# Performance work log

Measured on AMD Instinct MI355X. Metric: run time of the kernel, lower is better.

## Reference

```python
import jax, jax.numpy as jnp
import numpy as np

N = 50000          # atoms (nodes)
NEIGH = 12         # neighbors per atom
N_CRYS = 500       # crystals, 100 atoms each (contiguous)
H_E = 128          # h_fea_edge
H_A = 128          # h_fea_angle
N_CLS = 2
BOND_STEPS, BOND_MIN, BOND_MAX = 40, 0.0, 8.0
ANG_STEPS, ANG_MIN, ANG_MAX = 8, -1.0, 1.0


def _gbf(data, dmin, dmax, steps):
    # Gaussian basis expansion on the last (new) axis
    filters = jnp.linspace(dmin, dmax, steps, dtype=jnp.float32)
    gamma = (dmax - dmin) / steps
    return jnp.exp(-((data[..., None] - filters) ** 2) / (gamma ** 2))


def _sage_conv(x, src, dst, Wl, Wr, b):
    # PyG SAGEConv, mean aggregation:
    #   out_i = Wl @ mean_{(j->i) in E} x_j + b + Wr @ x_i
    n = x.shape[0]
    msg = x[src]                                             # [E, F] gather
    agg = jax.ops.segment_sum(msg, dst, num_segments=n)      # [N, F] scatter-add
    cnt = jax.ops.segment_sum(jnp.ones((src.shape[0],), x.dtype), dst, num_segments=n)
    agg = agg / jnp.maximum(cnt, 1.0)[:, None]
    return agg @ Wl.T + b + x @ Wr.T


def _segment_mean_pool(x, crys_idx):
    # crys_idx: [C, 2] contiguous [start, end) ranges covering [0, N)
    n = x.shape[0]
    starts = crys_idx[:, 0]
    seg_id = jnp.searchsorted(starts, jnp.arange(n), side='right') - 1
    counts = (crys_idx[:, 1] - crys_idx[:, 0]).astype(x.dtype)
    summed = jax.ops.segment_sum(x, seg_id, num_segments=crys_idx.shape[0])
    return summed / jnp.maximum(counts, 1.0)[:, None]


def setup_inputs() -> dict:
    key = jax.random.key(0)
    ks = jax.random.split(key, 24)
    in_b = BOND_STEPS * NEIGH            # 480
    in_a = ANG_STEPS * NEIGH * NEIGH     # 1152
    h_cat = H_E + H_A                    # 256

    def lin(k, fo, fi):
        return jax.random.normal(k, (fo, fi), jnp.float32) * (1.0 / np.sqrt(fi))

    atoms_per = N // N_CRYS
    starts = np.arange(N_CRYS, dtype=np.int32) * atoms_per
    crys_idx = jnp.asarray(np.stack([starts, starts + atoms_per], axis=1))

    return {
        'bond_fea': jax.random.uniform(ks[0], (N, NEIGH), jnp.float32) * BOND_MAX,
        'angle_fea': jax.random.uniform(ks[1], (N, NEIGH, NEIGH), jnp.float32) * 2.0 - 1.0,
        'species': jax.random.randint(ks[2], (N,), 0, 100, jnp.int32),
        'nbr_idx': jax.random.randint(ks[3], (N, NEIGH), 0, N, jnp.int32),
        'crys_idx': crys_idx,
        'Wl_b1': lin(ks[4], H_E, in_b), 'Wr_b1': lin(ks[5], H_E, in_b),
        'b_b1': jnp.zeros((H_E,), jnp.float32),
        'Wl_a1': lin(ks[6], H_A, in_a), 'Wr_a1': lin(ks[7], H_A, in_a),
        'b_a1': jnp.zeros((H_A,), jnp.float32),
        'Wl_b': jnp.stack([lin(ks[8], H_E, H_E), lin(ks[9], H_E, H_E)]),
        'Wr_b': jnp.stack([lin(ks[10], H_E, H_E), lin(ks[11], H_E, H_E)]),
        'b_b': jnp.zeros((2, H_E), jnp.float32),
        'Wl_a': jnp.stack([lin(ks[12], H_A, H_A), lin(ks[13], H_A, H_A)]),
        'Wr_a': jnp.stack([lin(ks[14], H_A, H_A), lin(ks[15], H_A, H_A)]),
        'b_a': jnp.zeros((2, H_A), jnp.float32),
        'W_mlp': jnp.stack([lin(ks[16], h_cat, h_cat), lin(ks[17], h_cat, h_cat)]),
        'b_mlp': jnp.zeros((2, h_cat), jnp.float32),
        'W_fc': lin(ks[18], N_CLS, h_cat),
        'b_fc': jnp.zeros((N_CLS,), jnp.float32),
    }


def reference(bond_fea, angle_fea, species, nbr_idx, crys_idx,
              Wl_b1, Wr_b1, b_b1, Wl_a1, Wr_a1, b_a1,
              Wl_b, Wr_b, b_b, Wl_a, Wr_a, b_a,
              W_mlp, b_mlp, W_fc, b_fc):
    n, neigh = nbr_idx.shape
    # get_edge_index: source = repeated node id, dest = neighbor id
    src = jnp.repeat(jnp.arange(n, dtype=nbr_idx.dtype), neigh)   # [N*neigh]
    dst = nbr_idx.reshape(-1)                                     # [N*neigh]

    # GBF expansions, flattened per node
    edge_fea = _gbf(bond_fea, BOND_MIN, BOND_MAX, BOND_STEPS).reshape(n, -1)    # [N, 480]
    ang_fea = _gbf(angle_fea, ANG_MIN, ANG_MAX, ANG_STEPS).reshape(n, -1)       # [N, 1152]

    # first SAGE layers (dropout_prob = 0 -> identity)
    b_out = jax.nn.relu(_sage_conv(edge_fea, src, dst, Wl_b1, Wr_b1, b_b1))
    a_out = jax.nn.relu(_sage_conv(ang_fea, src, dst, Wl_a1, Wr_a1, b_a1))

    # stacked SAGE layers (n_conv - 1 = 2 each)
    for i in range(Wl_b.shape[0]):
        b_out = jax.nn.relu(_sage_conv(b_out, src, dst, Wl_b[i], Wr_b[i], b_b[i]))
    for i in range(Wl_a.shape[0]):
        a_out = jax.nn.relu(_sage_conv(a_out, src, dst, Wl_a[i], Wr_a[i], b_a[i]))

    crys_fea = jnp.concatenate([b_out, a_out], axis=1)   # [N, 256]
    crys_fea = _segment_mean_pool(crys_fea, crys_idx)     # [C, 256]

    for i in range(W_mlp.shape[0]):
        crys_fea = crys_fea @ W_mlp[i].T + b_mlp[i]

    return crys_fea @ W_fc.T + b_fc                       # [C, n_classification]
```

## Files before the change

kernel.cpp:

```cpp
#include <hip/hip_runtime.h>

typedef _Float16 f16;
typedef _Float16 f16x8 __attribute__((ext_vector_type(8)));
typedef float f32x4 __attribute__((ext_vector_type(4)));

#define N_ATOMS 50000
#define NEIGH   12
#define NEDGE   (N_ATOMS * NEIGH)
#define NCRYS   500
#define NBLK    196

__device__ __forceinline__ void gld_lds16(const void* g, void* l) {
  __builtin_amdgcn_global_load_lds(
      (const __attribute__((address_space(1))) unsigned int*)g,
      (__attribute__((address_space(3))) unsigned int*)l, 16, 0, 0);
}

template <int MODE, int K>
__global__ __launch_bounds__(512) void gemm1(
    const float* __restrict__ Asrc, const f16* __restrict__ Wcat,
    f16* __restrict__ P, f16* __restrict__ Q, int n) {
  __shared__ __align__(16) f16 As[2][4][256][8];
  __shared__ __align__(16) f16 Bs[2][4][128][8];
  const int tid = threadIdx.x;
  const int lane = tid & 63;
  const int wid = tid >> 6;
  const int wr = wid >> 1;
  const int wc = wid & 1;
  const int row0 = blockIdx.x * 256;
  const int half = blockIdx.y;
  const f16* Wh = Wcat + (size_t)half * 128 * K;
  f16* outp = half ? Q : P;

  const int bcol = tid & 127;
  const int bkb = tid >> 7;
  const int sArow = tid & 255;
  const int sAkb0 = tid >> 8;
  int arow = row0 + sArow;
  if (arow >= n) arow = n - 1;

  f32x4 acc[4][4];
#pragma unroll
  for (int m = 0; m < 4; ++m)
#pragma unroll
    for (int q = 0; q < 4; ++q) acc[m][q] = (f32x4)0.f;

  auto stage = [&](int buf, int k0) {
    gld_lds16(Wh + (size_t)bcol * K + k0 + bkb * 8, &Bs[buf][bkb][bcol][0]);
#pragma unroll
    for (int p = 0; p < 2; ++p) {
      int kb = sAkb0 + 2 * p;
      int kg0 = k0 + kb * 8;
      f16 v[8];
      if constexpr (MODE == 1) {
        int jn = kg0 / 40;
        int kk0 = kg0 - jn * 40;
        float d = Asrc[arow * NEIGH + jn];
#pragma unroll
        for (int j = 0; j < 8; ++j) {
          float t = d - (kk0 + j) * (8.0f / 39.0f);
          v[j] = (f16)__expf(-t * t * 25.0f);
        }
      } else {
        int jn = kg0 >> 3;
        float d = Asrc[arow * 144 + jn];
#pragma unroll
        for (int j = 0; j < 8; ++j) {
          float t = d - (-1.0f + j * (2.0f / 7.0f));
          v[j] = (f16)__expf(-t * t * 16.0f);
        }
      }
      *(f16x8*)&As[buf][kb][sArow][0] = *(const f16x8*)v;
    }
  };

  constexpr int NT = K / 32;
  stage(0, 0);
  __syncthreads();
  int buf = 0;
  for (int t = 0; t < NT; ++t) {
    if (t + 1 < NT) stage(buf ^ 1, (t + 1) * 32);
    const int kb = lane >> 4;
    const int r16 = lane & 15;
    f16x8 a[4], b[4];
#pragma unroll
    for (int m = 0; m < 4; ++m)
      a[m] = *(const f16x8*)&As[buf][kb][wr * 64 + m * 16 + r16][0];
#pragma unroll
    for (int q = 0; q < 4; ++q)
      b[q] = *(const f16x8*)&Bs[buf][kb][wc * 64 + q * 16 + r16][0];
#pragma unroll
    for (int m = 0; m < 4; ++m)
#pragma unroll
      for (int q = 0; q < 4; ++q)
        acc[m][q] =
            __builtin_amdgcn_mfma_f32_16x16x32_f16(a[m], b[q], acc[m][q], 0, 0, 0);
    __syncthreads();
    buf ^= 1;
  }

  const int crow = (lane >> 4) * 4;
  const int ccol = lane & 15;
#pragma unroll
  for (int m = 0; m < 4; ++m) {
#pragma unroll
    for (int r = 0; r < 4; ++r) {
      int row = row0 + wr * 64 + m * 16 + crow + r;
      if (row < n) {
#pragma unroll
        for (int q = 0; q < 4; ++q)
          outp[(size_t)row * 128 + wc * 64 + q * 16 + ccol] = (f16)acc[m][q][r];
      }
    }
  }
}

__global__ __launch_bounds__(512) void gemmL(
    f16* __restrict__ axb, f16* __restrict__ axa, const f16* __restrict__ Wall,
    const float* __restrict__ bb, const float* __restrict__ ba, int lidx, int n) {
  __shared__ __align__(16) f16 As[2][4][256][8];
  __shared__ __align__(16) f16 Bs[2][4][128][8];
  const int path = blockIdx.y;
  f16* ax = path ? axa : axb;
  const f16* W = Wall + (size_t)(path * 2 + lidx) * 32768;
  const float* bias = (path ? ba : bb) + lidx * 128;

  const int tid = threadIdx.x;
  const int lane = tid & 63;
  const int wid = tid >> 6;
  const int wr = wid >> 1;
  const int wc = wid & 1;
  const int row0 = blockIdx.x * 256;

  const int bcol = tid & 127;
  const int bkb = tid >> 7;
  const int sArow = tid & 255;
  const int sAkb0 = tid >> 8;
  int arow = row0 + sArow;
  if (arow >= n) arow = n - 1;

  f32x4 acc[4][4];
#pragma unroll
  for (int m = 0; m < 4; ++m)
#pragma unroll
    for (int q = 0; q < 4; ++q) acc[m][q] = (f32x4)0.f;

  auto stage = [&](int buf, int k0) {
    gld_lds16(W + (size_t)bcol * 256 + k0 + bkb * 8, &Bs[buf][bkb][bcol][0]);
#pragma unroll
    for (int p = 0; p < 2; ++p) {
      int kb = sAkb0 + 2 * p;
      gld_lds16(ax + (size_t)arow * 256 + k0 + kb * 8, &As[buf][kb][sArow][0]);
    }
  };

  stage(0, 0);
  __syncthreads();
  int buf = 0;
  for (int t = 0; t < 8; ++t) {
    if (t + 1 < 8) stage(buf ^ 1, (t + 1) * 32);
    const int kb = lane >> 4;
    const int r16 = lane & 15;
    f16x8 a[4], b[4];
#pragma unroll
    for (int m = 0; m < 4; ++m)
      a[m] = *(const f16x8*)&As[buf][kb][wr * 64 + m * 16 + r16][0];
#pragma unroll
    for (int q = 0; q < 4; ++q)
      b[q] = *(const f16x8*)&Bs[buf][kb][wc * 64 + q * 16 + r16][0];
#pragma unroll
    for (int m = 0; m < 4; ++m)
#pragma unroll
      for (int q = 0; q < 4; ++q)
        acc[m][q] =
            __builtin_amdgcn_mfma_f32_16x16x32_f16(a[m], b[q], acc[m][q], 0, 0, 0);
    __syncthreads();
    buf ^= 1;
  }

  const int crow = (lane >> 4) * 4;
  const int ccol = lane & 15;
#pragma unroll
  for (int m = 0; m < 4; ++m) {
#pragma unroll
    for (int r = 0; r < 4; ++r) {
      int row = row0 + wr * 64 + m * 16 + crow + r;
      if (row < n) {
#pragma unroll
        for (int q = 0; q < 4; ++q) {
          int col = wc * 64 + q * 16 + ccol;
          float v = acc[m][q][r] + bias[col];
          ax[(size_t)row * 256 + 128 + col] = (f16)fmaxf(v, 0.0f);
        }
      }
    }
  }
}

__global__ void cvtW(const float* __restrict__ Wl, const float* __restrict__ Wr,
                     f16* __restrict__ outp, int K) {
  int c = blockIdx.y;
  int k = blockIdx.x * 256 + threadIdx.x;
  if (k < K)
    outp[(size_t)c * K + k] =
        (f16)((c < 128) ? Wl[(size_t)c * K + k] : Wr[(size_t)(c - 128) * K + k]);
}

__global__ void cvtW_small(const float* __restrict__ Wl_b, const float* __restrict__ Wr_b,
                           const float* __restrict__ Wl_a, const float* __restrict__ Wr_a,
                           f16* __restrict__ outp) {
  int idx = blockIdx.x * 256 + threadIdx.x;
  int l = idx >> 15;
  int c = (idx >> 8) & 127;
  int k = idx & 255;
  const float* Wl = (l < 2) ? Wl_b + (size_t)l * 16384 : Wl_a + (size_t)(l - 2) * 16384;
  const float* Wr = (l < 2) ? Wr_b + (size_t)l * 16384 : Wr_a + (size_t)(l - 2) * 16384;
  float v = (k < 128) ? Wl[(size_t)c * 128 + k] : Wr[(size_t)c * 128 + (k - 128)];
  outp[idx] = (f16)v;
}

__global__ void k_count(const int* __restrict__ nbr, int* __restrict__ deg) {
  int e = blockIdx.x * 256 + threadIdx.x;
  if (e < NEDGE) atomicAdd(&deg[nbr[e]], 1);
}
__global__ void k_scan1(const int* __restrict__ deg, int* __restrict__ rowptr,
                        int* __restrict__ bsum) {
  __shared__ int s[256];
  int t = threadIdx.x, i = blockIdx.x * 256 + t;
  int v = (i < N_ATOMS) ? deg[i] : 0;
  s[t] = v;
  __syncthreads();
  for (int off = 1; off < 256; off <<= 1) {
    int x = (t >= off) ? s[t - off] : 0;
    __syncthreads();
    s[t] += x;
    __syncthreads();
  }
  if (i < N_ATOMS) rowptr[i] = s[t] - v;
  if (t == 255) bsum[blockIdx.x] = s[255];
}
__global__ void k_scan2(int* __restrict__ bsum) {
  __shared__ int s[256];
  int t = threadIdx.x;
  int v = (t < NBLK) ? bsum[t] : 0;
  s[t] = v;
  __syncthreads();
  for (int off = 1; off < 256; off <<= 1) {
    int x = (t >= off) ? s[t - off] : 0;
    __syncthreads();
    s[t] += x;
    __syncthreads();
  }
  if (t < NBLK) bsum[t] = s[t] - v;
}
__global__ void k_scan3(int* __restrict__ rowptr, const int* __restrict__ bsum) {
  int i = blockIdx.x * 256 + threadIdx.x;
  if (i < N_ATOMS) rowptr[i] += bsum[blockIdx.x];
  if (i == 0) rowptr[N_ATOMS] = NEDGE;
}
__global__ void k_fill(const int* __restrict__ nbr, const int* __restrict__ rowptr,
                       int* __restrict__ cursor, int* __restrict__ eidx) {
  int e = blockIdx.x * 256 + threadIdx.x;
  if (e < NEDGE) {
    int dst = nbr[e];
    int pos = rowptr[dst] + atomicAdd(&cursor[dst], 1);
    eidx[pos] = e / NEIGH;
  }
}

__global__ __launch_bounds__(256) void gather_fin1(
    const f16* __restrict__ Pb, const f16* __restrict__ Qb,
    const f16* __restrict__ Pa, const f16* __restrict__ Qa,
    const int* __restrict__ rowptr, const int* __restrict__ eidx,
    const float* __restrict__ bias_b, const float* __restrict__ bias_a,
    f16* __restrict__ axb, f16* __restrict__ axa) {
  const int path = blockIdx.y;
  const f16* P = path ? Pa : Pb;
  const f16* Q = path ? Qa : Qb;
  const float* bias = path ? bias_a : bias_b;
  f16* ax = path ? axa : axb;
  const int t = threadIdx.x;
  const int a = blockIdx.x * 16 + (t >> 4);
  const int g = (t & 15) * 8;
  const int s0 = rowptr[a], s1 = rowptr[a + 1];
  float acc[8];
#pragma unroll
  for (int u = 0; u < 8; ++u) acc[u] = 0.f;
  int j = s0;
  for (; j + 4 <= s1; j += 4) {
    int src0 = eidx[j], src1 = eidx[j + 1], src2 = eidx[j + 2], src3 = eidx[j + 3];
    f16x8 v0 = *(const f16x8*)&P[(size_t)src0 * 128 + g];
    f16x8 v1 = *(const f16x8*)&P[(size_t)src1 * 128 + g];
    f16x8 v2 = *(const f16x8*)&P[(size_t)src2 * 128 + g];
    f16x8 v3 = *(const f16x8*)&P[(size_t)src3 * 128 + g];
#pragma unroll
    for (int u = 0; u < 8; ++u)
      acc[u] += ((float)v0[u] + (float)v1[u]) + ((float)v2[u] + (float)v3[u]);
  }
  for (; j < s1; ++j) {
    f16x8 v = *(const f16x8*)&P[(size_t)eidx[j] * 128 + g];
#pragma unroll
    for (int u = 0; u < 8; ++u) acc[u] += (float)v[u];
  }
  f16x8 q = *(const f16x8*)&Q[(size_t)a * 128 + g];
  float inv = 1.0f / fmaxf((float)(s1 - s0), 1.0f);
  f16 outv[8];
#pragma unroll
  for (int u = 0; u < 8; ++u) {
    float v = acc[u] * inv + bias[g + u] + (float)q[u];
    outv[u] = (f16)fmaxf(v, 0.0f);
  }
  *(f16x8*)&ax[(size_t)a * 256 + 128 + g] = *(const f16x8*)outv;
}

__global__ __launch_bounds__(256) void gather_mean(
    f16* __restrict__ axb, f16* __restrict__ axa,
    const int* __restrict__ rowptr, const int* __restrict__ eidx) {
  f16* ax = blockIdx.y ? axa : axb;
  const int t = threadIdx.x;
  const int a = blockIdx.x * 16 + (t >> 4);
  const int g = (t & 15) * 8;
  const int s0 = rowptr[a], s1 = rowptr[a + 1];
  float acc[8];
#pragma unroll
  for (int u = 0; u < 8; ++u) acc[u] = 0.f;
  int j = s0;
  for (; j + 4 <= s1; j += 4) {
    int src0 = eidx[j], src1 = eidx[j + 1], src2 = eidx[j + 2], src3 = eidx[j + 3];
    f16x8 v0 = *(const f16x8*)&ax[(size_t)src0 * 256 + 128 + g];
    f16x8 v1 = *(const f16x8*)&ax[(size_t)src1 * 256 + 128 + g];
    f16x8 v2 = *(const f16x8*)&ax[(size_t)src2 * 256 + 128 + g];
    f16x8 v3 = *(const f16x8*)&ax[(size_t)src3 * 256 + 128 + g];
#pragma unroll
    for (int u = 0; u < 8; ++u)
      acc[u] += ((float)v0[u] + (float)v1[u]) + ((float)v2[u] + (float)v3[u]);
  }
  for (; j < s1; ++j) {
    f16x8 v = *(const f16x8*)&ax[(size_t)eidx[j] * 256 + 128 + g];
#pragma unroll
    for (int u = 0; u < 8; ++u) acc[u] += (float)v[u];
  }
  float inv = 1.0f / fmaxf((float)(s1 - s0), 1.0f);
  f16 outv[8];
#pragma unroll
  for (int u = 0; u < 8; ++u) outv[u] = (f16)(acc[u] * inv);
  *(f16x8*)&ax[(size_t)a * 256 + g] = *(const f16x8*)outv;
}

__global__ __launch_bounds__(256) void head_kernel(
    const f16* __restrict__ axb, const f16* __restrict__ axa,
    const int* __restrict__ crys, const float* __restrict__ W_mlp,
    const float* __restrict__ b_mlp, const float* __restrict__ W_fc,
    const float* __restrict__ b_fc, float* __restrict__ outp) {
  __shared__ float sh0[256], sh1[256];
  const int cry = blockIdx.x, c = threadIdx.x;
  const int s = crys[2 * cry], e = crys[2 * cry + 1];
  const f16* src = (c < 128) ? axb : axa;
  const int ch = c & 127;
  float sum = 0.f;
  for (int r = s; r < e; ++r) sum += (float)src[(size_t)r * 256 + 128 + ch];
  sh0[c] = sum / fmaxf((float)(e - s), 1.0f);
  __syncthreads();
  {
    const float* wrow = W_mlp + (size_t)c * 256;
    float s2 = b_mlp[c];
#pragma unroll 8
    for (int k = 0; k < 256; k += 4) {
      float4 w = *(const float4*)&wrow[k];
      s2 += sh0[k] * w.x + sh0[k + 1] * w.y + sh0[k + 2] * w.z + sh0[k + 3] * w.w;
    }
    sh1[c] = s2;
  }
  __syncthreads();
  {
    const float* wrow = W_mlp + 65536 + (size_t)c * 256;
    float s2 = b_mlp[256 + c];
#pragma unroll 8
    for (int k = 0; k < 256; k += 4) {
      float4 w = *(const float4*)&wrow[k];
      s2 += sh1[k] * w.x + sh1[k + 1] * w.y + sh1[k + 2] * w.z + sh1[k + 3] * w.w;
    }
    sh0[c] = s2;
  }
  __syncthreads();
  if (c < 2) {
    const float* wrow = W_fc + c * 256;
    float s2 = b_fc[c];
    for (int k = 0; k < 256; ++k) s2 += sh0[k] * wrow[k];
    outp[cry * 2 + c] = s2;
  }
}

extern "C" void kernel_launch(void* const* d_in, const int* in_sizes, int n_in,
                              void* d_out, int out_size, void* d_ws, size_t ws_size,
                              hipStream_t stream) {
  const float* bond  = (const float*)d_in[0];
  const float* angle = (const float*)d_in[1];
  const int*   nbr   = (const int*)d_in[3];
  const int*   crys  = (const int*)d_in[4];
  const float* Wl_b1 = (const float*)d_in[5];
  const float* Wr_b1 = (const float*)d_in[6];
  const float* b_b1  = (const float*)d_in[7];
  const float* Wl_a1 = (const float*)d_in[8];
  const float* Wr_a1 = (const float*)d_in[9];
  const float* b_a1  = (const float*)d_in[10];
  const float* Wl_b  = (const float*)d_in[11];
  const float* Wr_b  = (const float*)d_in[12];
  const float* b_b   = (const float*)d_in[13];
  const float* Wl_a  = (const float*)d_in[14];
  const float* Wr_a  = (const float*)d_in[15];
  const float* b_a   = (const float*)d_in[16];
  const float* W_mlp = (const float*)d_in[17];
  const float* b_mlp = (const float*)d_in[18];
  const float* W_fc  = (const float*)d_in[19];
  const float* b_fc  = (const float*)d_in[20];

  char* w = (char*)d_ws;
  auto alloc = [&](size_t bytes) {
    void* p = (void*)w;
    w += (bytes + 255) & ~(size_t)255;
    return p;
  };
  f16* Pb   = (f16*)alloc((size_t)N_ATOMS * 128 * 2);
  f16* Qb   = (f16*)alloc((size_t)N_ATOMS * 128 * 2);
  f16* Pa   = (f16*)alloc((size_t)N_ATOMS * 128 * 2);
  f16* Qa   = (f16*)alloc((size_t)N_ATOMS * 128 * 2);
  f16* axb  = (f16*)alloc((size_t)N_ATOMS * 256 * 2);
  f16* axa  = (f16*)alloc((size_t)N_ATOMS * 256 * 2);
  f16* Wb1c = (f16*)alloc((size_t)256 * 480 * 2);
  f16* Wa1c = (f16*)alloc((size_t)256 * 1152 * 2);
  f16* Wsm  = (f16*)alloc((size_t)4 * 128 * 256 * 2);
  int* deg    = (int*)alloc((size_t)2 * N_ATOMS * 4);
  int* cursor = deg + N_ATOMS;
  int* rowptr = (int*)alloc((size_t)(N_ATOMS + 1) * 4);
  int* eidx   = (int*)alloc((size_t)NEDGE * 4);
  int* bsum   = (int*)alloc(256 * 4);

  cvtW<<<dim3(2, 256), 256, 0, stream>>>(Wl_b1, Wr_b1, Wb1c, 480);
  cvtW<<<dim3(5, 256), 256, 0, stream>>>(Wl_a1, Wr_a1, Wa1c, 1152);
  cvtW_small<<<512, 256, 0, stream>>>(Wl_b, Wr_b, Wl_a, Wr_a, Wsm);

  hipMemsetAsync(deg, 0, (size_t)2 * N_ATOMS * 4, stream);
  k_count<<<(NEDGE + 255) / 256, 256, 0, stream>>>(nbr, deg);
  k_scan1<<<NBLK, 256, 0, stream>>>(deg, rowptr, bsum);
  k_scan2<<<1, 256, 0, stream>>>(bsum);
  k_scan3<<<NBLK, 256, 0, stream>>>(rowptr, bsum);
  k_fill<<<(NEDGE + 255) / 256, 256, 0, stream>>>(nbr, rowptr, cursor, eidx);

  const int GT = (N_ATOMS + 255) / 256;
  const int AG = N_ATOMS / 16;

  gemm1<2, 1152><<<dim3(GT, 2), 512, 0, stream>>>(angle, Wa1c, Pa, Qa, N_ATOMS);
  gemm1<1, 480><<<dim3(GT, 2), 512, 0, stream>>>(bond, Wb1c, Pb, Qb, N_ATOMS);
  gather_fin1<<<dim3(AG, 2), 256, 0, stream>>>(Pb, Qb, Pa, Qa, rowptr, eidx,
                                               b_b1, b_a1, axb, axa);

  for (int l = 0; l < 2; ++l) {
    gather_mean<<<dim3(AG, 2), 256, 0, stream>>>(axb, axa, rowptr, eidx);
    gemmL<<<dim3(GT, 2), 512, 0, stream>>>(axb, axa, Wsm, b_b, b_a, l, N_ATOMS);
  }

  head_kernel<<<NCRYS, 256, 0, stream>>>(axb, axa, crys, W_mlp, b_mlp, W_fc, b_fc,
                                         (float*)d_out);
}
```

Before: 418.1 us.

## Replace LDS-staged GEMMs with register-direct MFMA loads and transposed inputs

Both first-layer and later GEMMs drop shared-memory double buffering and instead load A and B fragments directly from global memory into registers, prefetching one k-step ahead. The tile shrinks to 128 rows with 256 threads. Bond and angle inputs are first transposed to column-major so each lane's scalar loads coalesce across atoms. Later layers ping-pong between two activation buffers to avoid an in-place read/write hazard. This removes LDS traffic and barriers, at the cost of extra transpose kernels, redundant global loads of weights per wave, and more workspace.

```diff
diff --git a/kernel.cpp b/kernel.cpp
--- a/kernel.cpp
+++ b/kernel.cpp
@@ -10,34 +10,47 @@
 #define NCRYS   500
 #define NBLK    196
 
-__device__ __forceinline__ void gld_lds16(const void* g, void* l) {
-  __builtin_amdgcn_global_load_lds(
-      (const __attribute__((address_space(1))) unsigned int*)g,
-      (__attribute__((address_space(3))) unsigned int*)l, 16, 0, 0);
+template <int C>
+__global__ __launch_bounds__(256) void transposeT(const float* __restrict__ in,
+                                                  float* __restrict__ outp) {
+  __shared__ float tile[64 * C];
+  const int r0 = blockIdx.x * 64;
+  const int nr = min(64, N_ATOMS - r0);
+  for (int idx = threadIdx.x; idx < nr * C; idx += 256) {
+    int r = idx / C, c = idx - r * C;
+    tile[r * C + c] = in[(size_t)(r0 + r) * C + c];
+  }
+  __syncthreads();
+  for (int idx = threadIdx.x; idx < 64 * C; idx += 256) {
+    int c = idx >> 6, r = idx & 63;
+    if (r < nr) outp[(size_t)c * N_ATOMS + r0 + r] = tile[r * C + c];
+  }
 }
 
 template <int MODE, int K>
-__global__ __launch_bounds__(512) void gemm1(
-    const float* __restrict__ Asrc, const f16* __restrict__ Wcat,
+__global__ __launch_bounds__(256) void gemm1_reg(
+    const float* __restrict__ AT, const f16* __restrict__ Wcat,
     f16* __restrict__ P, f16* __restrict__ Q, int n) {
-  __shared__ __align__(16) f16 As[2][4][256][8];
-  __shared__ __align__(16) f16 Bs[2][4][128][8];
-  const int tid = threadIdx.x;
-  const int lane = tid & 63;
-  const int wid = tid >> 6;
-  const int wr = wid >> 1;
-  const int wc = wid & 1;
-  const int row0 = blockIdx.x * 256;
-  const int half = blockIdx.y;
-  const f16* Wh = Wcat + (size_t)half * 128 * K;
-  f16* outp = half ? Q : P;
-
-  const int bcol = tid & 127;
-  const int bkb = tid >> 7;
-  const int sArow = tid & 255;
-  const int sAkb0 = tid >> 8;
-  int arow = row0 + sArow;
-  if (arow >= n) arow = n - 1;
+  const int lane = threadIdx.x & 63;
+  const int wid = threadIdx.x >> 6;
+  const int wr = wid & 1;
+  const int wc = wid >> 1;
+  const int row0 = blockIdx.x * 128;
+  const f16* Wh = Wcat + (size_t)blockIdx.y * 128 * K;
+  f16* outp = blockIdx.y ? Q : P;
+  const int r16 = lane & 15;
+  const int kb = lane >> 4;
+
+  int rm[4];
+#pragma unroll
+  for (int m = 0; m < 4; ++m) {
+    int r = row0 + wr * 64 + m * 16 + r16;
+    rm[m] = (r < n) ? r : (n - 1);
+  }
+  const f16* wb[4];
+#pragma unroll
+  for (int q = 0; q < 4; ++q)
+    wb[q] = Wh + (size_t)(wc * 64 + q * 16 + r16) * K + kb * 8;
 
   f32x4 acc[4][4];
 #pragma unroll
@@ -45,58 +58,61 @@
 #pragma unroll
     for (int q = 0; q < 4; ++q) acc[m][q] = (f32x4)0.f;
 
-  auto stage = [&](int buf, int k0) {
-    gld_lds16(Wh + (size_t)bcol * K + k0 + bkb * 8, &Bs[buf][bkb][bcol][0]);
-#pragma unroll
-    for (int p = 0; p < 2; ++p) {
-      int kb = sAkb0 + 2 * p;
-      int kg0 = k0 + kb * 8;
-      f16 v[8];
-      if constexpr (MODE == 1) {
-        int jn = kg0 / 40;
-        int kk0 = kg0 - jn * 40;
-        float d = Asrc[arow * NEIGH + jn];
-#pragma unroll
-        for (int j = 0; j < 8; ++j) {
-          float t = d - (kk0 + j) * (8.0f / 39.0f);
-          v[j] = (f16)__expf(-t * t * 25.0f);
-        }
-      } else {
-        int jn = kg0 >> 3;
-        float d = Asrc[arow * 144 + jn];
-#pragma unroll
-        for (int j = 0; j < 8; ++j) {
-          float t = d - (-1.0f + j * (2.0f / 7.0f));
-          v[j] = (f16)__expf(-t * t * 16.0f);
-        }
+  constexpr int NT = K / 32;
+  float d0[4];
+  f16x8 b0[4];
+  {
+    int kg = kb * 8;
+    int jn = (MODE == 1) ? kg / 40 : (kg >> 3);
+#pragma unroll
+    for (int m = 0; m < 4; ++m) d0[m] = AT[(size_t)jn * N_ATOMS + rm[m]];
+#pragma unroll
+    for (int q = 0; q < 4; ++q) b0[q] = *(const f16x8*)(wb[q]);
+  }
+
+  for (int t = 0; t < NT; ++t) {
+    float d1[4];
+    f16x8 b1[4];
+    if (t + 1 < NT) {
+      int kg = (t + 1) * 32 + kb * 8;
+      int jn = (MODE == 1) ? kg / 40 : (kg >> 3);
+#pragma unroll
+      for (int m = 0; m < 4; ++m) d1[m] = AT[(size_t)jn * N_ATOMS + rm[m]];
+#pragma unroll
+      for (int q = 0; q < 4; ++q) b1[q] = *(const f16x8*)(wb[q] + (t + 1) * 32);
+    }
+    f16x8 a[4];
+    float fbase, fstep, g2i;
+    if constexpr (MODE == 1) {
+      int kg = t * 32 + kb * 8;
+      int jn = kg / 40;
+      fbase = (float)(kg - jn * 40) * (8.0f / 39.0f);
+      fstep = 8.0f / 39.0f;
+      g2i = 25.0f;
+    } else {
+      fbase = -1.0f;
+      fstep = 2.0f / 7.0f;
+      g2i = 16.0f;
+    }
+#pragma unroll
+    for (int m = 0; m < 4; ++m) {
+      float dd = d0[m];
+#pragma unroll
+      for (int j = 0; j < 8; ++j) {
+        float tt = dd - (fbase + (float)j * fstep);
+        a[m][j] = (f16)__expf(-tt * tt * g2i);
       }
-      *(f16x8*)&As[buf][kb][sArow][0] = *(const f16x8*)v;
-    }
-  };
-
-  constexpr int NT = K / 32;
-  stage(0, 0);
-  __syncthreads();
-  int buf = 0;
-  for (int t = 0; t < NT; ++t) {
-    if (t + 1 < NT) stage(buf ^ 1, (t + 1) * 32);
-    const int kb = lane >> 4;
-    const int r16 = lane & 15;
-    f16x8 a[4], b[4];
-#pragma unroll
-    for (int m = 0; m < 4; ++m)
-      a[m] = *(const f16x8*)&As[buf][kb][wr * 64 + m * 16 + r16][0];
-#pragma unroll
-    for (int q = 0; q < 4; ++q)
-      b[q] = *(const f16x8*)&Bs[buf][kb][wc * 64 + q * 16 + r16][0];
+    }
 #pragma unroll
     for (int m = 0; m < 4; ++m)
 #pragma unroll
       for (int q = 0; q < 4; ++q)
         acc[m][q] =
-            __builtin_amdgcn_mfma_f32_16x16x32_f16(a[m], b[q], acc[m][q], 0, 0, 0);
-    __syncthreads();
-    buf ^= 1;
+            __builtin_amdgcn_mfma_f32_16x16x32_f16(a[m], b0[q], acc[m][q], 0, 0, 0);
+#pragma unroll
+    for (int m = 0; m < 4; ++m) d0[m] = d1[m];
+#pragma unroll
+    for (int q = 0; q < 4; ++q) b0[q] = b1[q];
   }
 
   const int crow = (lane >> 4) * 4;
@@ -115,29 +131,34 @@
   }
 }
 
-__global__ __launch_bounds__(512) void gemmL(
-    f16* __restrict__ axb, f16* __restrict__ axa, const f16* __restrict__ Wall,
+__global__ __launch_bounds__(256) void gemmL_reg(
+    const f16* __restrict__ srcB, const f16* __restrict__ srcA,
+    f16* __restrict__ dstB, f16* __restrict__ dstA, const f16* __restrict__ Wall,
     const float* __restrict__ bb, const float* __restrict__ ba, int lidx, int n) {
-  __shared__ __align__(16) f16 As[2][4][256][8];
-  __shared__ __align__(16) f16 Bs[2][4][128][8];
   const int path = blockIdx.y;
-  f16* ax = path ? axa : axb;
+  const f16* src = path ? srcA : srcB;
+  f16* dst = path ? dstA : dstB;
   const f16* W = Wall + (size_t)(path * 2 + lidx) * 32768;
   const float* bias = (path ? ba : bb) + lidx * 128;
 
-  const int tid = threadIdx.x;
-  const int lane = tid & 63;
-  const int wid = tid >> 6;
-  const int wr = wid >> 1;
-  const int wc = wid & 1;
-  const int row0 = blockIdx.x * 256;
-
-  const int bcol = tid & 127;
-  const int bkb = tid >> 7;
-  const int sArow = tid & 255;
-  const int sAkb0 = tid >> 8;
-  int arow = row0 + sArow;
-  if (arow >= n) arow = n - 1;
+  const int lane = threadIdx.x & 63;
+  const int wid = threadIdx.x >> 6;
+  const int wr = wid & 1;
+  const int wc = wid >> 1;
+  const int row0 = blockIdx.x * 128;
+  const int r16 = lane & 15;
+  const int kb = lane >> 4;
+
+  int rm[4];
+#pragma unroll
+  for (int m = 0; m < 4; ++m) {
+    int r = row0 + wr * 64 + m * 16 + r16;
+    rm[m] = (r < n) ? r : (n - 1);
+  }
+  const f16* wb[4];
+#pragma unroll
+  for (int q = 0; q < 4; ++q)
+    wb[q] = W + (size_t)(wc * 64 + q * 16 + r16) * 256 + kb * 8;
 
   f32x4 acc[4][4];
 #pragma unroll
@@ -145,37 +166,33 @@
 #pragma unroll
     for (int q = 0; q < 4; ++q) acc[m][q] = (f32x4)0.f;
 
-  auto stage = [&](int buf, int k0) {
-    gld_lds16(W + (size_t)bcol * 256 + k0 + bkb * 8, &Bs[buf][bkb][bcol][0]);
-#pragma unroll
-    for (int p = 0; p < 2; ++p) {
-      int kb = sAkb0 + 2 * p;
-      gld_lds16(ax + (size_t)arow * 256 + k0 + kb * 8, &As[buf][kb][sArow][0]);
-    }
-  };
-
-  stage(0, 0);
-  __syncthreads();
-  int buf = 0;
+  f16x8 a0[4], b0[4];
+#pragma unroll
+  for (int m = 0; m < 4; ++m)
+    a0[m] = *(const f16x8*)&src[(size_t)rm[m] * 256 + kb * 8];
+#pragma unroll
+  for (int q = 0; q < 4; ++q) b0[q] = *(const f16x8*)(wb[q]);
+
   for (int t = 0; t < 8; ++t) {
-    if (t + 1 < 8) stage(buf ^ 1, (t + 1) * 32);
-    const int kb = lane >> 4;
-    const int r16 = lane & 15;
-    f16x8 a[4], b[4];
-#pragma unroll
-    for (int m = 0; m < 4; ++m)
-      a[m] = *(const f16x8*)&As[buf][kb][wr * 64 + m * 16 + r16][0];
-#pragma unroll
-    for (int q = 0; q < 4; ++q)
-      b[q] = *(const f16x8*)&Bs[buf][kb][wc * 64 + q * 16 + r16][0];
+    f16x8 a1[4], b1[4];
+    if (t + 1 < 8) {
+      int k = (t + 1) * 32 + kb * 8;
+#pragma unroll
+      for (int m = 0; m < 4; ++m)
+        a1[m] = *(const f16x8*)&src[(size_t)rm[m] * 256 + k];
+#pragma unroll
+      for (int q = 0; q < 4; ++q) b1[q] = *(const f16x8*)(wb[q] + (t + 1) * 32);
+    }
 #pragma unroll
     for (int m = 0; m < 4; ++m)
 #pragma unroll
       for (int q = 0; q < 4; ++q)
         acc[m][q] =
-            __builtin_amdgcn_mfma_f32_16x16x32_f16(a[m], b[q], acc[m][q], 0, 0, 0);
-    __syncthreads();
-    buf ^= 1;
+            __builtin_amdgcn_mfma_f32_16x16x32_f16(a0[m], b0[q], acc[m][q], 0, 0, 0);
+#pragma unroll
+    for (int m = 0; m < 4; ++m) a0[m] = a1[m];
+#pragma unroll
+    for (int q = 0; q < 4; ++q) b0[q] = b1[q];
   }
 
   const int crow = (lane >> 4) * 4;
@@ -190,7 +207,7 @@
         for (int q = 0; q < 4; ++q) {
           int col = wc * 64 + q * 16 + ccol;
           float v = acc[m][q][r] + bias[col];
-          ax[(size_t)row * 256 + 128 + col] = (f16)fmaxf(v, 0.0f);
+          dst[(size_t)row * 256 + 128 + col] = (f16)fmaxf(v, 0.0f);
         }
       }
     }
@@ -421,12 +438,16 @@
     w += (bytes + 255) & ~(size_t)255;
     return p;
   };
-  f16* Pb   = (f16*)alloc((size_t)N_ATOMS * 128 * 2);
-  f16* Qb   = (f16*)alloc((size_t)N_ATOMS * 128 * 2);
-  f16* Pa   = (f16*)alloc((size_t)N_ATOMS * 128 * 2);
-  f16* Qa   = (f16*)alloc((size_t)N_ATOMS * 128 * 2);
-  f16* axb  = (f16*)alloc((size_t)N_ATOMS * 256 * 2);
-  f16* axa  = (f16*)alloc((size_t)N_ATOMS * 256 * 2);
+  f16* axbA = (f16*)alloc((size_t)N_ATOMS * 256 * 2);
+  f16* axaA = (f16*)alloc((size_t)N_ATOMS * 256 * 2);
+  f16* axbB = (f16*)alloc((size_t)N_ATOMS * 256 * 2);
+  f16* axaB = (f16*)alloc((size_t)N_ATOMS * 256 * 2);
+  f16* Pb = axbB;
+  f16* Qb = axbB + (size_t)N_ATOMS * 128;
+  f16* Pa = axaB;
+  f16* Qa = axaB + (size_t)N_ATOMS * 128;
+  float* angleT = (float*)alloc((size_t)144 * N_ATOMS * 4);
+  float* bondT  = (float*)alloc((size_t)12 * N_ATOMS * 4);
   f16* Wb1c = (f16*)alloc((size_t)256 * 480 * 2);
   f16* Wa1c = (f16*)alloc((size_t)256 * 1152 * 2);
   f16* Wsm  = (f16*)alloc((size_t)4 * 128 * 256 * 2);
@@ -436,6 +457,11 @@
   int* eidx   = (int*)alloc((size_t)NEDGE * 4);
   int* bsum   = (int*)alloc(256 * 4);
 
+  const int TT = (N_ATOMS + 63) / 64;
+
+  transposeT<144><<<TT, 256, 0, stream>>>(angle, angleT);
+  transposeT<12><<<TT, 256, 0, stream>>>(bond, bondT);
+
   cvtW<<<dim3(2, 256), 256, 0, stream>>>(Wl_b1, Wr_b1, Wb1c, 480);
   cvtW<<<dim3(5, 256), 256, 0, stream>>>(Wl_a1, Wr_a1, Wa1c, 1152);
   cvtW_small<<<512, 256, 0, stream>>>(Wl_b, Wr_b, Wl_a, Wr_a, Wsm);
@@ -447,19 +473,21 @@
   k_scan3<<<NBLK, 256, 0, stream>>>(rowptr, bsum);
   k_fill<<<(NEDGE + 255) / 256, 256, 0, stream>>>(nbr, rowptr, cursor, eidx);
 
-  const int GT = (N_ATOMS + 255) / 256;
+  const int GG = (N_ATOMS + 127) / 128;
   const int AG = N_ATOMS / 16;
 
-  gemm1<2, 1152><<<dim3(GT, 2), 512, 0, stream>>>(angle, Wa1c, Pa, Qa, N_ATOMS);
-  gemm1<1, 480><<<dim3(GT, 2), 512, 0, stream>>>(bond, Wb1c, Pb, Qb, N_ATOMS);
+  gemm1_reg<2, 1152><<<dim3(GG, 2), 256, 0, stream>>>(angleT, Wa1c, Pa, Qa, N_ATOMS);
+  gemm1_reg<1, 480><<<dim3(GG, 2), 256, 0, stream>>>(bondT, Wb1c, Pb, Qb, N_ATOMS);
   gather_fin1<<<dim3(AG, 2), 256, 0, stream>>>(Pb, Qb, Pa, Qa, rowptr, eidx,
-                                               b_b1, b_a1, axb, axa);
-
-  for (int l = 0; l < 2; ++l) {
-    gather_mean<<<dim3(AG, 2), 256, 0, stream>>>(axb, axa, rowptr, eidx);
-    gemmL<<<dim3(GT, 2), 512, 0, stream>>>(axb, axa, Wsm, b_b, b_a, l, N_ATOMS);
-  }
-
-  head_kernel<<<NCRYS, 256, 0, stream>>>(axb, axa, crys, W_mlp, b_mlp, W_fc, b_fc,
+                                               b_b1, b_a1, axbA, axaA);
+
+  gather_mean<<<dim3(AG, 2), 256, 0, stream>>>(axbA, axaA, rowptr, eidx);
+  gemmL_reg<<<dim3(GG, 2), 256, 0, stream>>>(axbA, axaA, axbB, axaB, Wsm, b_b, b_a,
+                                             0, N_ATOMS);
+  gather_mean<<<dim3(AG, 2), 256, 0, stream>>>(axbB, axaB, rowptr, eidx);
+  gemmL_reg<<<dim3(GG, 2), 256, 0, stream>>>(axbB, axaB, axbA, axaA, Wsm, b_b, b_a,
+                                             1, N_ATOMS);
+
+  head_kernel<<<NCRYS, 256, 0, stream>>>(axbA, axaA, crys, W_mlp, b_mlp, W_fc, b_fc,
                                          (float*)d_out);
 }
```

Measured after the change: 479.1 us. +14.6%, slower.

## Use register-direct GEMM with ping-pong buffers and byte-offset edge gather

Applied to the files above, without the earlier changes.

Replaces the LDS double-buffered layer GEMM with a 256-thread kernel that loads A and W fragments straight from global memory into registers. It writes output into a separate ping-pong buffer so in-place hazards disappear and no block barriers are needed. Edge indices are stored pre-shifted as byte offsets, and the gather kernels add an 8-wide unrolled loop with packed fp16 vector adds before converting to fp32. The aim is less LDS traffic, less synchronisation, fewer address computations and more gather memory-level parallelism. The cost is reduced fp16 accumulation precision within groups and uncoalesced-ish direct global loads in the GEMM.

```diff
diff --git a/kernel.cpp b/kernel.cpp
--- a/kernel.cpp
+++ b/kernel.cpp
@@ -115,29 +115,34 @@
   }
 }
 
-__global__ __launch_bounds__(512) void gemmL(
-    f16* __restrict__ axb, f16* __restrict__ axa, const f16* __restrict__ Wall,
+__global__ __launch_bounds__(256) void gemmL_reg(
+    const f16* __restrict__ srcB, const f16* __restrict__ srcA,
+    f16* __restrict__ dstB, f16* __restrict__ dstA, const f16* __restrict__ Wall,
     const float* __restrict__ bb, const float* __restrict__ ba, int lidx, int n) {
-  __shared__ __align__(16) f16 As[2][4][256][8];
-  __shared__ __align__(16) f16 Bs[2][4][128][8];
   const int path = blockIdx.y;
-  f16* ax = path ? axa : axb;
+  const f16* src = path ? srcA : srcB;
+  f16* dst = path ? dstA : dstB;
   const f16* W = Wall + (size_t)(path * 2 + lidx) * 32768;
   const float* bias = (path ? ba : bb) + lidx * 128;
 
-  const int tid = threadIdx.x;
-  const int lane = tid & 63;
-  const int wid = tid >> 6;
-  const int wr = wid >> 1;
-  const int wc = wid & 1;
-  const int row0 = blockIdx.x * 256;
-
-  const int bcol = tid & 127;
-  const int bkb = tid >> 7;
-  const int sArow = tid & 255;
-  const int sAkb0 = tid >> 8;
-  int arow = row0 + sArow;
-  if (arow >= n) arow = n - 1;
+  const int lane = threadIdx.x & 63;
+  const int wid = threadIdx.x >> 6;
+  const int wr = wid & 1;
+  const int wc = wid >> 1;
+  const int row0 = blockIdx.x * 128;
+  const int r16 = lane & 15;
+  const int kb = lane >> 4;
+
+  int rm[4];
+#pragma unroll
+  for (int m = 0; m < 4; ++m) {
+    int r = row0 + wr * 64 + m * 16 + r16;
+    rm[m] = (r < n) ? r : (n - 1);
+  }
+  const f16* wb[4];
+#pragma unroll
+  for (int q = 0; q < 4; ++q)
+    wb[q] = W + (size_t)(wc * 64 + q * 16 + r16) * 256 + kb * 8;
 
   f32x4 acc[4][4];
 #pragma unroll
@@ -145,37 +150,20 @@
 #pragma unroll
     for (int q = 0; q < 4; ++q) acc[m][q] = (f32x4)0.f;
 
-  auto stage = [&](int buf, int k0) {
-    gld_lds16(W + (size_t)bcol * 256 + k0 + bkb * 8, &Bs[buf][bkb][bcol][0]);
-#pragma unroll
-    for (int p = 0; p < 2; ++p) {
-      int kb = sAkb0 + 2 * p;
-      gld_lds16(ax + (size_t)arow * 256 + k0 + kb * 8, &As[buf][kb][sArow][0]);
-    }
-  };
-
-  stage(0, 0);
-  __syncthreads();
-  int buf = 0;
+#pragma unroll
   for (int t = 0; t < 8; ++t) {
-    if (t + 1 < 8) stage(buf ^ 1, (t + 1) * 32);
-    const int kb = lane >> 4;
-    const int r16 = lane & 15;
     f16x8 a[4], b[4];
 #pragma unroll
     for (int m = 0; m < 4; ++m)
-      a[m] = *(const f16x8*)&As[buf][kb][wr * 64 + m * 16 + r16][0];
-#pragma unroll
-    for (int q = 0; q < 4; ++q)
-      b[q] = *(const f16x8*)&Bs[buf][kb][wc * 64 + q * 16 + r16][0];
+      a[m] = *(const f16x8*)&src[(size_t)rm[m] * 256 + t * 32 + kb * 8];
+#pragma unroll
+    for (int q = 0; q < 4; ++q) b[q] = *(const f16x8*)(wb[q] + t * 32);
 #pragma unroll
     for (int m = 0; m < 4; ++m)
 #pragma unroll
       for (int q = 0; q < 4; ++q)
         acc[m][q] =
             __builtin_amdgcn_mfma_f32_16x16x32_f16(a[m], b[q], acc[m][q], 0, 0, 0);
-    __syncthreads();
-    buf ^= 1;
   }
 
   const int crow = (lane >> 4) * 4;
@@ -190,7 +178,7 @@
         for (int q = 0; q < 4; ++q) {
           int col = wc * 64 + q * 16 + ccol;
           float v = acc[m][q][r] + bias[col];
-          ax[(size_t)row * 256 + 128 + col] = (f16)fmaxf(v, 0.0f);
+          dst[(size_t)row * 256 + 128 + col] = (f16)fmaxf(v, 0.0f);
         }
       }
     }
@@ -264,7 +252,7 @@
   if (e < NEDGE) {
     int dst = nbr[e];
     int pos = rowptr[dst] + atomicAdd(&cursor[dst], 1);
-    eidx[pos] = e / NEIGH;
+    eidx[pos] = (e / NEIGH) << 8;
   }
 }
 
@@ -275,32 +263,41 @@
     const float* __restrict__ bias_b, const float* __restrict__ bias_a,
     f16* __restrict__ axb, f16* __restrict__ axa) {
   const int path = blockIdx.y;
-  const f16* P = path ? Pa : Pb;
+  const char* Pc = (const char*)(path ? Pa : Pb);
   const f16* Q = path ? Qa : Qb;
   const float* bias = path ? bias_a : bias_b;
   f16* ax = path ? axa : axb;
   const int t = threadIdx.x;
   const int a = blockIdx.x * 16 + (t >> 4);
   const int g = (t & 15) * 8;
+  const unsigned gb = (unsigned)(t & 15) * 16;
   const int s0 = rowptr[a], s1 = rowptr[a + 1];
   float acc[8];
 #pragma unroll
   for (int u = 0; u < 8; ++u) acc[u] = 0.f;
   int j = s0;
+  for (; j + 8 <= s1; j += 8) {
+    f16x8 v[8];
+#pragma unroll
+    for (int u = 0; u < 8; ++u)
+      v[u] = *(const f16x8*)(Pc + (size_t)((unsigned)eidx[j + u] + gb));
+    f16x8 s = ((v[0] + v[1]) + (v[2] + v[3])) + ((v[4] + v[5]) + (v[6] + v[7]));
+#pragma unroll
+    for (int c = 0; c < 8; ++c) acc[c] += (float)s[c];
+  }
   for (; j + 4 <= s1; j += 4) {
-    int src0 = eidx[j], src1 = eidx[j + 1], src2 = eidx[j + 2], src3 = eidx[j + 3];
-    f16x8 v0 = *(const f16x8*)&P[(size_t)src0 * 128 + g];
-    f16x8 v1 = *(const f16x8*)&P[(size_t)src1 * 128 + g];
-    f16x8 v2 = *(const f16x8*)&P[(size_t)src2 * 128 + g];
-    f16x8 v3 = *(const f16x8*)&P[(size_t)src3 * 128 + g];
-#pragma unroll
-    for (int u = 0; u < 8; ++u)
-      acc[u] += ((float)v0[u] + (float)v1[u]) + ((float)v2[u] + (float)v3[u]);
+    f16x8 v0 = *(const f16x8*)(Pc + (size_t)((unsigned)eidx[j] + gb));
+    f16x8 v1 = *(const f16x8*)(Pc + (size_t)((unsigned)eidx[j + 1] + gb));
+    f16x8 v2 = *(const f16x8*)(Pc + (size_t)((unsigned)eidx[j + 2] + gb));
+    f16x8 v3 = *(const f16x8*)(Pc + (size_t)((unsigned)eidx[j + 3] + gb));
+    f16x8 s = (v0 + v1) + (v2 + v3);
+#pragma unroll
+    for (int c = 0; c < 8; ++c) acc[c] += (float)s[c];
   }
   for (; j < s1; ++j) {
-    f16x8 v = *(const f16x8*)&P[(size_t)eidx[j] * 128 + g];
-#pragma unroll
-    for (int u = 0; u < 8; ++u) acc[u] += (float)v[u];
+    f16x8 v = *(const f16x8*)(Pc + (size_t)((unsigned)eidx[j] + gb));
+#pragma unroll
+    for (int c = 0; c < 8; ++c) acc[c] += (float)v[c];
   }
   f16x8 q = *(const f16x8*)&Q[(size_t)a * 128 + g];
   float inv = 1.0f / fmaxf((float)(s1 - s0), 1.0f);
@@ -317,28 +314,38 @@
     f16* __restrict__ axb, f16* __restrict__ axa,
     const int* __restrict__ rowptr, const int* __restrict__ eidx) {
   f16* ax = blockIdx.y ? axa : axb;
+  const char* axc = (const char*)ax;
   const int t = threadIdx.x;
   const int a = blockIdx.x * 16 + (t >> 4);
   const int g = (t & 15) * 8;
+  const unsigned gb = 256u + (unsigned)(t & 15) * 16;
   const int s0 = rowptr[a], s1 = rowptr[a + 1];
   float acc[8];
 #pragma unroll
   for (int u = 0; u < 8; ++u) acc[u] = 0.f;
   int j = s0;
+  for (; j + 8 <= s1; j += 8) {
+    f16x8 v[8];
+#pragma unroll
+    for (int u = 0; u < 8; ++u)
+      v[u] = *(const f16x8*)(axc + (size_t)(((unsigned)eidx[j + u] << 1) + gb));
+    f16x8 s = ((v[0] + v[1]) + (v[2] + v[3])) + ((v[4] + v[5]) + (v[6] + v[7]));
+#pragma unroll
+    for (int c = 0; c < 8; ++c) acc[c] += (float)s[c];
+  }
   for (; j + 4 <= s1; j += 4) {
-    int src0 = eidx[j], src1 = eidx[j + 1], src2 = eidx[j + 2], src3 = eidx[j + 3];
-    f16x8 v0 = *(const f16x8*)&ax[(size_t)src0 * 256 + 128 + g];
-    f16x8 v1 = *(const f16x8*)&ax[(size_t)src1 * 256 + 128 + g];
-    f16x8 v2 = *(const f16x8*)&ax[(size_t)src2 * 256 + 128 + g];
-    f16x8 v3 = *(const f16x8*)&ax[(size_t)src3 * 256 + 128 + g];
-#pragma unroll
-    for (int u = 0; u < 8; ++u)
-      acc[u] += ((float)v0[u] + (float)v1[u]) + ((float)v2[u] + (float)v3[u]);
+    f16x8 v0 = *(const f16x8*)(axc + (size_t)(((unsigned)eidx[j] << 1) + gb));
+    f16x8 v1 = *(const f16x8*)(axc + (size_t)(((unsigned)eidx[j + 1] << 1) + gb));
+    f16x8 v2 = *(const f16x8*)(axc + (size_t)(((unsigned)eidx[j + 2] << 1) + gb));
+    f16x8 v3 = *(const f16x8*)(axc + (size_t)(((unsigned)eidx[j + 3] << 1) + gb));
+    f16x8 s = (v0 + v1) + (v2 + v3);
+#pragma unroll
+    for (int c = 0; c < 8; ++c) acc[c] += (float)s[c];
   }
   for (; j < s1; ++j) {
-    f16x8 v = *(const f16x8*)&ax[(size_t)eidx[j] * 256 + 128 + g];
-#pragma unroll
-    for (int u = 0; u < 8; ++u) acc[u] += (float)v[u];
+    f16x8 v = *(const f16x8*)(axc + (size_t)(((unsigned)eidx[j] << 1) + gb));
+#pragma unroll
+    for (int c = 0; c < 8; ++c) acc[c] += (float)v[c];
   }
   float inv = 1.0f / fmaxf((float)(s1 - s0), 1.0f);
   f16 outv[8];
@@ -421,12 +428,14 @@
     w += (bytes + 255) & ~(size_t)255;
     return p;
   };
-  f16* Pb   = (f16*)alloc((size_t)N_ATOMS * 128 * 2);
-  f16* Qb   = (f16*)alloc((size_t)N_ATOMS * 128 * 2);
-  f16* Pa   = (f16*)alloc((size_t)N_ATOMS * 128 * 2);
-  f16* Qa   = (f16*)alloc((size_t)N_ATOMS * 128 * 2);
-  f16* axb  = (f16*)alloc((size_t)N_ATOMS * 256 * 2);
-  f16* axa  = (f16*)alloc((size_t)N_ATOMS * 256 * 2);
+  f16* axbA = (f16*)alloc((size_t)N_ATOMS * 256 * 2);
+  f16* axaA = (f16*)alloc((size_t)N_ATOMS * 256 * 2);
+  f16* axbB = (f16*)alloc((size_t)N_ATOMS * 256 * 2);
+  f16* axaB = (f16*)alloc((size_t)N_ATOMS * 256 * 2);
+  f16* Pb = axbB;
+  f16* Qb = axbB + (size_t)N_ATOMS * 128;
+  f16* Pa = axaB;
+  f16* Qa = axaB + (size_t)N_ATOMS * 128;
   f16* Wb1c = (f16*)alloc((size_t)256 * 480 * 2);
   f16* Wa1c = (f16*)alloc((size_t)256 * 1152 * 2);
   f16* Wsm  = (f16*)alloc((size_t)4 * 128 * 256 * 2);
@@ -448,18 +457,21 @@
   k_fill<<<(NEDGE + 255) / 256, 256, 0, stream>>>(nbr, rowptr, cursor, eidx);
 
   const int GT = (N_ATOMS + 255) / 256;
+  const int GG = (N_ATOMS + 127) / 128;
   const int AG = N_ATOMS / 16;
 
   gemm1<2, 1152><<<dim3(GT, 2), 512, 0, stream>>>(angle, Wa1c, Pa, Qa, N_ATOMS);
   gemm1<1, 480><<<dim3(GT, 2), 512, 0, stream>>>(bond, Wb1c, Pb, Qb, N_ATOMS);
   gather_fin1<<<dim3(AG, 2), 256, 0, stream>>>(Pb, Qb, Pa, Qa, rowptr, eidx,
-                                               b_b1, b_a1, axb, axa);
-
-  for (int l = 0; l < 2; ++l) {
-    gather_mean<<<dim3(AG, 2), 256, 0, stream>>>(axb, axa, rowptr, eidx);
-    gemmL<<<dim3(GT, 2), 512, 0, stream>>>(axb, axa, Wsm, b_b, b_a, l, N_ATOMS);
-  }
-
-  head_kernel<<<NCRYS, 256, 0, stream>>>(axb, axa, crys, W_mlp, b_mlp, W_fc, b_fc,
+                                               b_b1, b_a1, axbA, axaA);
+
+  gather_mean<<<dim3(AG, 2), 256, 0, stream>>>(axbA, axaA, rowptr, eidx);
+  gemmL_reg<<<dim3(GG, 2), 256, 0, stream>>>(axbA, axaA, axbB, axaB, Wsm, b_b, b_a,
+                                             0, N_ATOMS);
+  gather_mean<<<dim3(AG, 2), 256, 0, stream>>>(axbB, axaB, rowptr, eidx);
+  gemmL_reg<<<dim3(GG, 2), 256, 0, stream>>>(axbB, axaB, axbA, axaA, Wsm, b_b, b_a,
+                                             1, N_ATOMS);
+
+  head_kernel<<<NCRYS, 256, 0, stream>>>(axbA, axaA, crys, W_mlp, b_mlp, W_fc, b_fc,
                                          (float*)d_out);
 }
```

Measured after the change: 442.5 us. +5.8%, slower.

## Merge first-layer GEMMs into one launch and use byte-offset f16 gathers

Applied to the files above, without the earlier changes.

Both first-layer GEMMs (angle and bond) now run in a single launch, selected by blockIdx.z, so the smaller bond GEMM can fill the machine alongside the angle GEMM. The edge index array now stores premultiplied byte offsets (src<<8), which removes index multiplies in the gather kernels. The gathers are unrolled to eight neighbours and do the partial sums in packed f16 before converting to f32. The f16 partial sums of up to eight values lose some precision, and the byte offsets held in 32-bit unsigned limit how large the node count can be.

```diff
diff --git a/kernel.cpp b/kernel.cpp
--- a/kernel.cpp
+++ b/kernel.cpp
@@ -16,12 +16,13 @@
       (__attribute__((address_space(3))) unsigned int*)l, 16, 0, 0);
 }
 
+typedef f16 AsT[2][4][256][8];
+typedef f16 BsT[2][4][128][8];
+
 template <int MODE, int K>
-__global__ __launch_bounds__(512) void gemm1(
+__device__ __forceinline__ void gemm1_body(
     const float* __restrict__ Asrc, const f16* __restrict__ Wcat,
-    f16* __restrict__ P, f16* __restrict__ Q, int n) {
-  __shared__ __align__(16) f16 As[2][4][256][8];
-  __shared__ __align__(16) f16 Bs[2][4][128][8];
+    f16* __restrict__ P, f16* __restrict__ Q, int n, AsT& As, BsT& Bs) {
   const int tid = threadIdx.x;
   const int lane = tid & 63;
   const int wid = tid >> 6;
@@ -115,11 +116,24 @@
   }
 }
 
+__global__ __launch_bounds__(512) void gemm1all(
+    const float* __restrict__ angle, const f16* __restrict__ Wa,
+    f16* __restrict__ Pa, f16* __restrict__ Qa,
+    const float* __restrict__ bond, const f16* __restrict__ Wb,
+    f16* __restrict__ Pb, f16* __restrict__ Qb, int n) {
+  __shared__ __align__(16) AsT As;
+  __shared__ __align__(16) BsT Bs;
+  if (blockIdx.z == 0)
+    gemm1_body<2, 1152>(angle, Wa, Pa, Qa, n, As, Bs);
+  else
+    gemm1_body<1, 480>(bond, Wb, Pb, Qb, n, As, Bs);
+}
+
 __global__ __launch_bounds__(512) void gemmL(
     f16* __restrict__ axb, f16* __restrict__ axa, const f16* __restrict__ Wall,
     const float* __restrict__ bb, const float* __restrict__ ba, int lidx, int n) {
-  __shared__ __align__(16) f16 As[2][4][256][8];
-  __shared__ __align__(16) f16 Bs[2][4][128][8];
+  __shared__ __align__(16) AsT As;
+  __shared__ __align__(16) BsT Bs;
   const int path = blockIdx.y;
   f16* ax = path ? axa : axb;
   const f16* W = Wall + (size_t)(path * 2 + lidx) * 32768;
@@ -264,7 +278,7 @@
   if (e < NEDGE) {
     int dst = nbr[e];
     int pos = rowptr[dst] + atomicAdd(&cursor[dst], 1);
-    eidx[pos] = e / NEIGH;
+    eidx[pos] = (e / NEIGH) << 8;
   }
 }
 
@@ -275,32 +289,41 @@
     const float* __restrict__ bias_b, const float* __restrict__ bias_a,
     f16* __restrict__ axb, f16* __restrict__ axa) {
   const int path = blockIdx.y;
-  const f16* P = path ? Pa : Pb;
+  const char* Pc = (const char*)(path ? Pa : Pb);
   const f16* Q = path ? Qa : Qb;
   const float* bias = path ? bias_a : bias_b;
   f16* ax = path ? axa : axb;
   const int t = threadIdx.x;
   const int a = blockIdx.x * 16 + (t >> 4);
   const int g = (t & 15) * 8;
+  const unsigned gb = (unsigned)(t & 15) * 16;
   const int s0 = rowptr[a], s1 = rowptr[a + 1];
   float acc[8];
 #pragma unroll
   for (int u = 0; u < 8; ++u) acc[u] = 0.f;
   int j = s0;
+  for (; j + 8 <= s1; j += 8) {
+    f16x8 v[8];
+#pragma unroll
+    for (int u = 0; u < 8; ++u)
+      v[u] = *(const f16x8*)(Pc + (size_t)((unsigned)eidx[j + u] + gb));
+    f16x8 s = ((v[0] + v[1]) + (v[2] + v[3])) + ((v[4] + v[5]) + (v[6] + v[7]));
+#pragma unroll
+    for (int c = 0; c < 8; ++c) acc[c] += (float)s[c];
+  }
   for (; j + 4 <= s1; j += 4) {
-    int src0 = eidx[j], src1 = eidx[j + 1], src2 = eidx[j + 2], src3 = eidx[j + 3];
-    f16x8 v0 = *(const f16x8*)&P[(size_t)src0 * 128 + g];
-    f16x8 v1 = *(const f16x8*)&P[(size_t)src1 * 128 + g];
-    f16x8 v2 = *(const f16x8*)&P[(size_t)src2 * 128 + g];
-    f16x8 v3 = *(const f16x8*)&P[(size_t)src3 * 128 + g];
-#pragma unroll
-    for (int u = 0; u < 8; ++u)
-      acc[u] += ((float)v0[u] + (float)v1[u]) + ((float)v2[u] + (float)v3[u]);
+    f16x8 v0 = *(const f16x8*)(Pc + (size_t)((unsigned)eidx[j] + gb));
+    f16x8 v1 = *(const f16x8*)(Pc + (size_t)((unsigned)eidx[j + 1] + gb));
+    f16x8 v2 = *(const f16x8*)(Pc + (size_t)((unsigned)eidx[j + 2] + gb));
+    f16x8 v3 = *(const f16x8*)(Pc + (size_t)((unsigned)eidx[j + 3] + gb));
+    f16x8 s = (v0 + v1) + (v2 + v3);
+#pragma unroll
+    for (int c = 0; c < 8; ++c) acc[c] += (float)s[c];
   }
   for (; j < s1; ++j) {
-    f16x8 v = *(const f16x8*)&P[(size_t)eidx[j] * 128 + g];
-#pragma unroll
-    for (int u = 0; u < 8; ++u) acc[u] += (float)v[u];
+    f16x8 v = *(const f16x8*)(Pc + (size_t)((unsigned)eidx[j] + gb));
+#pragma unroll
+    for (int c = 0; c < 8; ++c) acc[c] += (float)v[c];
   }
   f16x8 q = *(const f16x8*)&Q[(size_t)a * 128 + g];
   float inv = 1.0f / fmaxf((float)(s1 - s0), 1.0f);
@@ -317,28 +340,38 @@
     f16* __restrict__ axb, f16* __restrict__ axa,
     const int* __restrict__ rowptr, const int* __restrict__ eidx) {
   f16* ax = blockIdx.y ? axa : axb;
+  const char* axc = (const char*)ax;
   const int t = threadIdx.x;
   const int a = blockIdx.x * 16 + (t >> 4);
   const int g = (t & 15) * 8;
+  const unsigned gb = 256u + (unsigned)(t & 15) * 16;
   const int s0 = rowptr[a], s1 = rowptr[a + 1];
   float acc[8];
 #pragma unroll
   for (int u = 0; u < 8; ++u) acc[u] = 0.f;
   int j = s0;
+  for (; j + 8 <= s1; j += 8) {
+    f16x8 v[8];
+#pragma unroll
+    for (int u = 0; u < 8; ++u)
+      v[u] = *(const f16x8*)(axc + (size_t)(((unsigned)eidx[j + u] << 1) + gb));
+    f16x8 s = ((v[0] + v[1]) + (v[2] + v[3])) + ((v[4] + v[5]) + (v[6] + v[7]));
+#pragma unroll
+    for (int c = 0; c < 8; ++c) acc[c] += (float)s[c];
+  }
   for (; j + 4 <= s1; j += 4) {
-    int src0 = eidx[j], src1 = eidx[j + 1], src2 = eidx[j + 2], src3 = eidx[j + 3];
-    f16x8 v0 = *(const f16x8*)&ax[(size_t)src0 * 256 + 128 + g];
-    f16x8 v1 = *(const f16x8*)&ax[(size_t)src1 * 256 + 128 + g];
-    f16x8 v2 = *(const f16x8*)&ax[(size_t)src2 * 256 + 128 + g];
-    f16x8 v3 = *(const f16x8*)&ax[(size_t)src3 * 256 + 128 + g];
-#pragma unroll
-    for (int u = 0; u < 8; ++u)
-      acc[u] += ((float)v0[u] + (float)v1[u]) + ((float)v2[u] + (float)v3[u]);
+    f16x8 v0 = *(const f16x8*)(axc + (size_t)(((unsigned)eidx[j] << 1) + gb));
+    f16x8 v1 = *(const f16x8*)(axc + (size_t)(((unsigned)eidx[j + 1] << 1) + gb));
+    f16x8 v2 = *(const f16x8*)(axc + (size_t)(((unsigned)eidx[j + 2] << 1) + gb));
+    f16x8 v3 = *(const f16x8*)(axc + (size_t)(((unsigned)eidx[j + 3] << 1) + gb));
+    f16x8 s = (v0 + v1) + (v2 + v3);
+#pragma unroll
+    for (int c = 0; c < 8; ++c) acc[c] += (float)s[c];
   }
   for (; j < s1; ++j) {
-    f16x8 v = *(const f16x8*)&ax[(size_t)eidx[j] * 256 + 128 + g];
-#pragma unroll
-    for (int u = 0; u < 8; ++u) acc[u] += (float)v[u];
+    f16x8 v = *(const f16x8*)(axc + (size_t)(((unsigned)eidx[j] << 1) + gb));
+#pragma unroll
+    for (int c = 0; c < 8; ++c) acc[c] += (float)v[c];
   }
   float inv = 1.0f / fmaxf((float)(s1 - s0), 1.0f);
   f16 outv[8];
@@ -421,12 +454,12 @@
     w += (bytes + 255) & ~(size_t)255;
     return p;
   };
-  f16* Pb   = (f16*)alloc((size_t)N_ATOMS * 128 * 2);
-  f16* Qb   = (f16*)alloc((size_t)N_ATOMS * 128 * 2);
-  f16* Pa   = (f16*)alloc((size_t)N_ATOMS * 128 * 2);
-  f16* Qa   = (f16*)alloc((size_t)N_ATOMS * 128 * 2);
-  f16* axb  = (f16*)alloc((size_t)N_ATOMS * 256 * 2);
-  f16* axa  = (f16*)alloc((size_t)N_ATOMS * 256 * 2);
+  f16* axb = (f16*)alloc((size_t)N_ATOMS * 256 * 2);
+  f16* axa = (f16*)alloc((size_t)N_ATOMS * 256 * 2);
+  f16* Pb  = (f16*)alloc((size_t)N_ATOMS * 128 * 2);
+  f16* Qb  = (f16*)alloc((size_t)N_ATOMS * 128 * 2);
+  f16* Pa  = (f16*)alloc((size_t)N_ATOMS * 128 * 2);
+  f16* Qa  = (f16*)alloc((size_t)N_ATOMS * 128 * 2);
   f16* Wb1c = (f16*)alloc((size_t)256 * 480 * 2);
   f16* Wa1c = (f16*)alloc((size_t)256 * 1152 * 2);
   f16* Wsm  = (f16*)alloc((size_t)4 * 128 * 256 * 2);
@@ -450,8 +483,8 @@
   const int GT = (N_ATOMS + 255) / 256;
   const int AG = N_ATOMS / 16;
 
-  gemm1<2, 1152><<<dim3(GT, 2), 512, 0, stream>>>(angle, Wa1c, Pa, Qa, N_ATOMS);
-  gemm1<1, 480><<<dim3(GT, 2), 512, 0, stream>>>(bond, Wb1c, Pb, Qb, N_ATOMS);
+  gemm1all<<<dim3(GT, 2, 2), 512, 0, stream>>>(angle, Wa1c, Pa, Qa,
+                                               bond, Wb1c, Pb, Qb, N_ATOMS);
   gather_fin1<<<dim3(AG, 2), 256, 0, stream>>>(Pb, Qb, Pa, Qa, rowptr, eidx,
                                                b_b1, b_a1, axb, axa);
 
```

New measurement: 405.4 us. -3.0%, faster.
